# Performance work log

Measured on AMD Instinct MI355X. Metric: run time of the kernel, lower is better.

Reference implementation:

```python
import jax, jax.numpy as jnp
import numpy as np
from functools import partial

EPS = 1e-5

def batchnorm(x, gamma, beta):
    # training-mode BN over (N,H,W) per channel, NCHW layout
    mean = jnp.mean(x, axis=(0, 2, 3), keepdims=True)
    var = jnp.var(x, axis=(0, 2, 3), keepdims=True)
    xn = (x - mean) * jax.lax.rsqrt(var + EPS)
    return xn * gamma[None, :, None, None] + beta[None, :, None, None]

def ternarize(w):
    # TBN-style per-output-filter ternary quantization: {-a,0,+a}
    absw = jnp.abs(w)
    delta = 0.7 * jnp.mean(absw, axis=(1, 2, 3), keepdims=True)
    mask = (absw > delta).astype(w.dtype)
    alpha = jnp.sum(absw * mask, axis=(1, 2, 3), keepdims=True) / (
        jnp.sum(mask, axis=(1, 2, 3), keepdims=True) + 1e-8)
    return jnp.sign(w) * mask * alpha

def conv(x, w, stride, padding):
    return jax.lax.conv_general_dilated(
        x, w, window_strides=(stride, stride),
        padding=[(padding, padding), (padding, padding)],
        dimension_numbers=("NCHW", "OIHW", "NCHW"))


def setup_inputs() -> dict:
    key = jax.random.key(0)
    ks = jax.random.split(key, 8)
    in_planes, planes, stride = 512, 256, 2
    out_planes = planes * 4
    d = dict(
        x=jax.random.normal(ks[0], (64, in_planes, 28, 28), dtype=jnp.float32),
        bn1_g=jnp.ones((in_planes,), jnp.float32),
        bn1_b=jnp.zeros((in_planes,), jnp.float32),
        w1=jax.random.normal(ks[1], (planes, in_planes, 1, 1), jnp.float32) * 0.05,
        bn2_g=jnp.ones((planes,), jnp.float32),
        bn2_b=jnp.zeros((planes,), jnp.float32),
        w2=jax.random.normal(ks[2], (planes, planes, 3, 3), jnp.float32) * 0.05,
        bn3_g=jnp.ones((planes,), jnp.float32),
        bn3_b=jnp.zeros((planes,), jnp.float32),
        w3=jax.random.normal(ks[3], (out_planes, planes, 1, 1), jnp.float32) * 0.05,
        ds_w=jax.random.normal(ks[4], (out_planes, in_planes, 1, 1), jnp.float32) * 0.05,
        ds_bn_g=jnp.ones((out_planes,), jnp.float32),
        ds_bn_b=jnp.zeros((out_planes,), jnp.float32),
    )
    return d


def reference(x, bn1_g, bn1_b, w1, bn2_g, bn2_b, w2, bn3_g, bn3_b, w3,
              ds_w, ds_bn_g, ds_bn_b):
    stride = 2
    identity = x
    # pre-activation chain: BN -> ternary-quantized conv
    h = conv(batchnorm(x, bn1_g, bn1_b), ternarize(w1), 1, 0)          # [N,256,28,28]
    h = conv(batchnorm(h, bn2_g, bn2_b), ternarize(w2), stride, 1)     # [N,256,14,14]
    h = conv(batchnorm(h, bn3_g, bn3_b), ternarize(w3), 1, 0)          # [N,1024,14,14]
    # downsample(identity, x): projected shortcut + residual add
    sc = batchnorm(conv(identity, ds_w, stride, 0), ds_bn_g, ds_bn_b)
    return h + sc
```

## Files before the change

### kernel.cpp

```cpp
#include <hip/hip_runtime.h>
#include <hip/hip_bf16.h>
#include <math.h>

#define EPS 1e-5f

typedef __hip_bfloat16 bf16;
typedef short short8 __attribute__((ext_vector_type(8)));
typedef float float4v __attribute__((ext_vector_type(4)));

__device__ __forceinline__ float toF(float v) { return v; }
__device__ __forceinline__ float toF(bf16 v) { return __bfloat162float(v); }
__device__ __forceinline__ void stF(float* p, float v) { *p = v; }
__device__ __forceinline__ void stF(bf16* p, float v) { *p = __float2bfloat16(v); }
__device__ __forceinline__ short f2bs(float v) {
    bf16 b = __float2bfloat16(v);
    return *reinterpret_cast<short*>(&b);
}
__device__ __forceinline__ float bs2f(short s) {
    unsigned u = ((unsigned)(unsigned short)s) << 16;
    return __uint_as_float(u);
}

__device__ __forceinline__ void gload_lds16(const short* g, short* l) {
    __builtin_amdgcn_global_load_lds(
        (const __attribute__((address_space(1))) unsigned int*)g,
        (__attribute__((address_space(3))) unsigned int*)l, 16, 0, 0);
}

__device__ __forceinline__ void bn_fin(float sum, float sq, float g, float b, float cnt,
                                       float& scale, float& shift) {
    float mean = sum / cnt;
    float var = fmaxf(sq / cnt - mean * mean, 0.f);
    float r = rsqrtf(var + EPS);
    scale = g * r;
    shift = b - mean * scale;
}

__device__ __forceinline__ float block_reduce_sum(float v) {
    __shared__ float s[256];
    int t = threadIdx.x;
    s[t] = v;
    __syncthreads();
    #pragma unroll
    for (int st = 128; st > 0; st >>= 1) {
        if (t < st) s[t] += s[t + st];
        __syncthreads();
    }
    float r = s[0];
    __syncthreads();
    return r;
}

__device__ __forceinline__ void ternarize_body(const float* __restrict__ w,
                                               short* __restrict__ wt,
                                               float* __restrict__ alpha, int K, int f) {
    const float* wf = w + (size_t)f * K;
    short* wtf = wt + (size_t)f * K;

    float s = 0.f;
    for (int i = threadIdx.x; i < K; i += 256) s += fabsf(wf[i]);
    float total = block_reduce_sum(s);
    float delta = 0.7f * total / (float)K;

    float sm = 0.f, cm = 0.f;
    for (int i = threadIdx.x; i < K; i += 256) {
        float a = fabsf(wf[i]);
        if (a > delta) { sm += a; cm += 1.f; }
    }
    sm = block_reduce_sum(sm);
    cm = block_reduce_sum(cm);
    if (threadIdx.x == 0) alpha[f] = sm / (cm + 1e-8f);

    for (int i = threadIdx.x; i < K; i += 256) {
        float v = wf[i];
        float a = fabsf(v);
        wtf[i] = (a > delta) ? ((v > 0.f) ? (short)0x3F80 : (short)0xBF80) : (short)0;
    }
}

__global__ __launch_bounds__(256) void prep_kernel(
    const float* __restrict__ w1, const float* __restrict__ w2,
    const float* __restrict__ w3, const float* __restrict__ ds_w,
    short* __restrict__ w1t, short* __restrict__ w2t, short* __restrict__ w3t,
    short* __restrict__ dswb,
    float* __restrict__ alpha1, float* __restrict__ alpha2, float* __restrict__ alpha3,
    const float* __restrict__ x, short* __restrict__ B1t,
    float* __restrict__ sum1, float* __restrict__ sq1) {
    int b = blockIdx.x;
    if (b < 256)        ternarize_body(w1, w1t, alpha1, 512, b);
    else if (b < 512)   ternarize_body(w2, w2t, alpha2, 2304, b - 256);
    else if (b < 1536)  ternarize_body(w3, w3t, alpha3, 256, b - 512);
    else if (b < 3584) {
        int i = (b - 1536) * 256 + threadIdx.x;
        if (i < 1024 * 512) dswb[i] = f2bs(ds_w[i]);
    } else {
        const int C = 512, SP = 784;
        __shared__ short tile[64][66];
        __shared__ float rs[4][64], rq[4][64];
        int bb = b - 3584;
        int n = bb / 104;
        int ci0 = ((bb / 13) % 8) * 64;
        int p0 = (bb % 13) * 64;
        int t = threadIdx.x;
        int tx = t & 63;
        int ty4 = t >> 6;

        {
            int p4 = t & 15;
            int cib = t >> 4;
            int p = p0 + p4 * 4;
            bool pok = (p + 3) < SP;
            #pragma unroll
            for (int it = 0; it < 4; it++) {
                int ci = cib + it * 16;
                float4 q;
                if (pok) q = *(const float4*)(x + ((size_t)n * C + ci0 + ci) * SP + p);
                else     q = make_float4(0.f, 0.f, 0.f, 0.f);
                tile[p4 * 4 + 0][ci] = f2bs(q.x);
                tile[p4 * 4 + 1][ci] = f2bs(q.y);
                tile[p4 * 4 + 2][ci] = f2bs(q.z);
                tile[p4 * 4 + 3][ci] = f2bs(q.w);
            }
        }
        __syncthreads();

        {
            int seg = t & 7;
            #pragma unroll
            for (int it = 0; it < 2; it++) {
                int pl = (t >> 3) + it * 32;
                int pw = p0 + pl;
                if (pw < SP) {
                    short v[8];
                    #pragma unroll
                    for (int u = 0; u < 8; u++) v[u] = tile[pl][seg * 8 + u];
                    *(int4*)(B1t + ((size_t)n * SP + pw) * C + ci0 + seg * 8) = *(int4*)v;
                }
            }
        }

        float s = 0.f, s2 = 0.f;
        #pragma unroll
        for (int r = 0; r < 16; r++) {
            int pl = ty4 + r * 4;
            int pw = p0 + pl;
            if (pw < SP) {
                float v = bs2f(tile[pl][tx]);
                s += v; s2 += v * v;
            }
        }
        rs[ty4][tx] = s; rq[ty4][tx] = s2;
        __syncthreads();
        if (ty4 == 0) {
            float ts = rs[0][tx] + rs[1][tx] + rs[2][tx] + rs[3][tx];
            float tq = rq[0][tx] + rq[1][tx] + rq[2][tx] + rq[3][tx];
            atomicAdd(&sum1[ci0 + tx], ts);
            atomicAdd(&sq1[ci0 + tx], tq);
        }
    }
}

__global__ void foldbias_kernel(const short* __restrict__ wt,
                                const float* __restrict__ sum, const float* __restrict__ sq,
                                const float* __restrict__ g, const float* __restrict__ b,
                                short* __restrict__ wf, float* __restrict__ bias,
                                int K, float cnt) {
    int f = blockIdx.x;
    float s = 0.f;
    for (int k = threadIdx.x; k < K; k += blockDim.x) {
        float scale, shift;
        bn_fin(sum[k], sq[k], g[k], b[k], cnt, scale, shift);
        float tv = bs2f(wt[(size_t)f * K + k]);
        wf[(size_t)f * K + k] = f2bs(tv * scale);
        s += tv * shift;
    }
    s = block_reduce_sum(s);
    if (threadIdx.x == 0) bias[f] = s;
}

template <typename T, int VEC>
__global__ __launch_bounds__(256) void bn_sum_kernel(
    const T* __restrict__ src, float* __restrict__ sum, float* __restrict__ sq,
    int C, int spatial, int N, int splits) {
    int c = blockIdx.x;
    int vpc = spatial / VEC;
    int total = N * vpc;
    float s = 0.f, s2 = 0.f;
    for (int v = blockIdx.y * 256 + threadIdx.x; v < total; v += splits * 256) {
        int n = v / vpc;
        int i = v - n * vpc;
        const T* p = src + ((size_t)n * C + c) * spatial + i * VEC;
        short tmp[VEC];
        if (VEC == 8) *(int4*)tmp = *(const int4*)p;
        else          *(int2*)tmp = *(const int2*)p;
        #pragma unroll
        for (int k = 0; k < VEC; k++) { float vv = bs2f(tmp[k]); s += vv; s2 += vv * vv; }
    }
    s = block_reduce_sum(s);
    s2 = block_reduce_sum(s2);
    if (threadIdx.x == 0) {
        atomicAdd(&sum[c], s);
        atomicAdd(&sq[c], s2);
    }
}

template <int VEC>
__device__ __forceinline__ void bn_sum_body(const bf16* __restrict__ src, int C, int c,
                                            int spatial, int N, int splits,
                                            float* __restrict__ sum, float* __restrict__ sq) {
    int vpc = spatial / VEC;
    int total = N * vpc;
    float s = 0.f, s2 = 0.f;
    for (int v = blockIdx.y * 256 + threadIdx.x; v < total; v += splits * 256) {
        int n = v / vpc;
        int i = v - n * vpc;
        const bf16* p = src + ((size_t)n * C + c) * spatial + i * VEC;
        short tmp[VEC];
        if (VEC == 8) *(int4*)tmp = *(const int4*)p;
        else          *(int2*)tmp = *(const int2*)p;
        #pragma unroll
        for (int k = 0; k < VEC; k++) { float vv = bs2f(tmp[k]); s += vv; s2 += vv * vv; }
    }
    s = block_reduce_sum(s);
    s2 = block_reduce_sum(s2);
    if (threadIdx.x == 0) {
        atomicAdd(&sum[c], s);
        atomicAdd(&sq[c], s2);
    }
}

__global__ __launch_bounds__(256) void bn_sum_dual_kernel(
    const bf16* __restrict__ scv, const bf16* __restrict__ h1,
    float* __restrict__ sumd, float* __restrict__ sqd,
    float* __restrict__ sum2, float* __restrict__ sq2) {
    int cb = blockIdx.x;
    if (cb < 1024) bn_sum_body<4>(scv, 1024, cb, 196, 64, 8, sumd, sqd);
    else           bn_sum_body<8>(h1, 256, cb - 1024, 784, 64, 8, sum2, sq2);
}

__global__ __launch_bounds__(256) void affine_transpose_bf16_kernel(
    const bf16* __restrict__ in,
    const float* __restrict__ sum, const float* __restrict__ sq,
    const float* __restrict__ g, const float* __restrict__ b, float cnt,
    short* __restrict__ Bt, int C, int SP) {
    __shared__ short tile[64][66];
    int n = blockIdx.z;
    int ci0 = blockIdx.y * 64;
    int p0 = blockIdx.x * 64;
    int t = threadIdx.x;

    {
        int p4 = t & 15;
        int cib = t >> 4;
        int p = p0 + p4 * 4;
        bool pok = (p + 3) < SP;
        #pragma unroll
        for (int it = 0; it < 4; it++) {
            int ci = cib + it * 16;
            short v[4] = {0, 0, 0, 0};
            if (pok) *(int2*)v = *(const int2*)(in + ((size_t)n * C + ci0 + ci) * SP + p);
            float sc, sh;
            bn_fin(sum[ci0 + ci], sq[ci0 + ci], g[ci0 + ci], b[ci0 + ci], cnt, sc, sh);
            #pragma unroll
            for (int j = 0; j < 4; j++)
                tile[p4 * 4 + j][ci] = f2bs(bs2f(v[j]) * sc + sh);
        }
    }
    __syncthreads();

    {
        int seg = t & 7;
        #pragma unroll
        for (int it = 0; it < 2; it++) {
            int pl = (t >> 3) + it * 32;
            int pw = p0 + pl;
            if (pw < SP) {
                short v[8];
                #pragma unroll
                for (int u = 0; u < 8; u++) v[u] = tile[pl][seg * 8 + u];
                *(int4*)(Bt + ((size_t)n * SP + pw) * C + ci0 + seg * 8) = *(int4*)v;
            }
        }
    }
}

__global__ __launch_bounds__(256) void im2col_tiled_kernel(
    const bf16* __restrict__ h1,
    const float* __restrict__ sum, const float* __restrict__ sq,
    const float* __restrict__ g, const float* __restrict__ b, float cnt,
    short* __restrict__ B2t) {
    __shared__ short tile[16][784];
    int cb = blockIdx.x;
    int n  = blockIdx.y;
    int ci0 = cb * 16;
    int t = threadIdx.x;

    for (int v = t; v < 16 * 98; v += 256) {
        int ci = v / 98;
        int i8 = (v - ci * 98) * 8;
        short tmp[8];
        *(int4*)tmp = *(const int4*)(h1 + ((size_t)n * 256 + ci0 + ci) * 784 + i8);
        float sc, sh;
        bn_fin(sum[ci0 + ci], sq[ci0 + ci], g[ci0 + ci], b[ci0 + ci], cnt, sc, sh);
        short ov[8];
        #pragma unroll
        for (int k = 0; k < 8; k++) ov[k] = f2bs(bs2f(tmp[k]) * sc + sh);
        *(int4*)&tile[ci][i8] = *(int4*)ov;
    }
    __syncthreads();

    for (int w = t; w < 196 * 18; w += 256) {
        int p = w / 18, seg = w - p * 18;
        int oh = p / 14, ow = p - oh * 14;
        int kbase = seg * 8;
        short vals[8];
        #pragma unroll
        for (int u = 0; u < 8; u++) {
            int kk = kbase + u;
            int ci_l = kk / 9;
            int rr = kk - ci_l * 9;
            int kh = rr / 3, kw = rr - kh * 3;
            int ih = 2 * oh - 1 + kh;
            int iw = 2 * ow - 1 + kw;
            vals[u] = ((unsigned)ih < 28u && (unsigned)iw < 28u)
                          ? tile[ci_l][ih * 28 + iw] : (short)0;
        }
        *(int4*)(B2t + ((size_t)(n * 196 + p)) * 2304 + ci0 * 9 + kbase) = *(int4*)vals;
    }
}

__global__ __launch_bounds__(256) void gemm14_kernel(
    const short* __restrict__ w1f, const short* __restrict__ dswb,
    const short* __restrict__ B1t,
    const float* __restrict__ alpha1, const float* __restrict__ bias1,
    bf16* __restrict__ h1, bf16* __restrict__ sc) {
    int blk = blockIdx.x;
    int t = threadIdx.x;
    int w = t >> 6, l = t & 63;
    int r0 = t >> 2;
    int kg = (t & 3) * 8;
    int wbase = w * 512;
    int lm = (l >> 4);
    int lc = l & 15;

    if (blk < 784) {
        __shared__ short As[128 * 32];
        __shared__ short Bs[128 * 32];
        const int SP = 784, M = 256, K = 512;
        int c0 = (blk / 2) * 128;
        int m0 = (blk % 2) * 128;
        int wm = (w >> 1) * 64, wn = (w & 1) * 64;
        size_t rowB0 = c0 + r0;
        size_t rowB1 = c0 + r0 + 64;

        float4v acc[4][4];
        #pragma unroll
        for (int i = 0; i < 4; i++)
            #pragma unroll
            for (int j = 0; j < 4; j++) acc[i][j] = (float4v)0.f;

        for (int k0 = 0; k0 < K; k0 += 32) {
            gload_lds16(w1f + (size_t)(m0 + r0) * K + k0 + kg,      &As[wbase]);
            gload_lds16(w1f + (size_t)(m0 + r0 + 64) * K + k0 + kg, &As[2048 + wbase]);
            gload_lds16(B1t + rowB0 * K + k0 + kg,                  &Bs[wbase]);
            gload_lds16(B1t + rowB1 * K + k0 + kg,                  &Bs[2048 + wbase]);
            __syncthreads();

            short8 af[4], bfr[4];
            #pragma unroll
            for (int i = 0; i < 4; i++)
                af[i] = *(const short8*)&As[(wm + i * 16 + lc) * 32 + lm * 8];
            #pragma unroll
            for (int j = 0; j < 4; j++)
                bfr[j] = *(const short8*)&Bs[(wn + j * 16 + lc) * 32 + lm * 8];
            #pragma unroll
            for (int i = 0; i < 4; i++)
                #pragma unroll
                for (int j = 0; j < 4; j++)
                    acc[i][j] = __builtin_amdgcn_mfma_f32_16x16x32_bf16(af[i], bfr[j], acc[i][j], 0, 0, 0);
            __syncthreads();
        }

        #pragma unroll
        for (int i = 0; i < 4; i++) {
            #pragma unroll
            for (int r = 0; r < 4; r++) {
                int m = m0 + wm + i * 16 + lm * 4 + r;
                float a = alpha1[m];
                float bia = bias1[m];
                #pragma unroll
                for (int j = 0; j < 4; j++) {
                    int c = c0 + wn + j * 16 + lc;
                    int n = c / SP;
                    int p = c - n * SP;
                    h1[((size_t)n * M + m) * SP + p] = __float2bfloat16((acc[i][j][r] + bia) * a);
                }
            }
        }
    } else {
        __shared__ short As4[64 * 32];
        __shared__ short Bs4[64 * 32];
        const int SP = 196, M = 1024, K = 512;
        int bb = blk - 784;
        int c0 = (bb / 16) * 64;
        int m0 = (bb % 16) * 64;
        int wm = (w >> 1) * 32, wn = (w & 1) * 32;

        int c = c0 + r0;
        int nn = c / 196, pp = c - nn * 196;
        int oh = pp / 14, ow = pp - oh * 14;
        size_t rowB = (size_t)nn * 784 + oh * 56 + ow * 2;

        float4v acc[2][2];
        #pragma unroll
        for (int i = 0; i < 2; i++)
            #pragma unroll
            for (int j = 0; j < 2; j++) acc[i][j] = (float4v)0.f;

        for (int k0 = 0; k0 < K; k0 += 32) {
            gload_lds16(dswb + (size_t)(m0 + r0) * K + k0 + kg, &As4[wbase]);
            gload_lds16(B1t + rowB * K + k0 + kg,               &Bs4[wbase]);
            __syncthreads();

            short8 af[2], bfr[2];
            #pragma unroll
            for (int i = 0; i < 2; i++)
                af[i] = *(const short8*)&As4[(wm + i * 16 + lc) * 32 + lm * 8];
            #pragma unroll
            for (int j = 0; j < 2; j++)
                bfr[j] = *(const short8*)&Bs4[(wn + j * 16 + lc) * 32 + lm * 8];
            #pragma unroll
            for (int i = 0; i < 2; i++)
                #pragma unroll
                for (int j = 0; j < 2; j++)
                    acc[i][j] = __builtin_amdgcn_mfma_f32_16x16x32_bf16(af[i], bfr[j], acc[i][j], 0, 0, 0);
            __syncthreads();
        }

        #pragma unroll
        for (int i = 0; i < 2; i++) {
            #pragma unroll
            for (int r = 0; r < 4; r++) {
                int m = m0 + wm + i * 16 + lm * 4 + r;
                #pragma unroll
                for (int j = 0; j < 2; j++) {
                    int cc = c0 + wn + j * 16 + lc;
                    int n = cc / SP;
                    int p = cc - n * SP;
                    sc[((size_t)n * M + m) * SP + p] = __float2bfloat16(acc[i][j][r]);
                }
            }
        }
    }
}

template <int SP, typename TOut, bool HAS_ALPHA, bool FUSE, bool HAS_BIAS, bool BREMAP>
__global__ __launch_bounds__(256) void gemm_kernel(
    const short* __restrict__ A, const short* __restrict__ Bt,
    const float* __restrict__ alpha, TOut* __restrict__ out,
    int M, int K,
    const bf16* __restrict__ scv,
    const float* __restrict__ fsum, const float* __restrict__ fsq,
    const float* __restrict__ fg, const float* __restrict__ fb, float fcnt,
    const float* __restrict__ bias) {
    __shared__ short As[128 * 32];
    __shared__ short Bs[128 * 32];
    int t = threadIdx.x;
    int c0 = blockIdx.x * 128;
    int m0 = blockIdx.y * 128;
    int w = t >> 6, l = t & 63;
    int wm = (w >> 1) * 64, wn = (w & 1) * 64;

    int r0 = t >> 2;
    int kg = (t & 3) * 8;
    int wbase = w * 512;

    size_t rowB0, rowB1;
    if (BREMAP) {
        int c = c0 + r0;
        int nn = c / 196, pp = c - nn * 196;
        int oh = pp / 14, ow = pp - oh * 14;
        rowB0 = (size_t)nn * 784 + oh * 56 + ow * 2;
        c += 64;
        nn = c / 196; pp = c - nn * 196;
        oh = pp / 14; ow = pp - oh * 14;
        rowB1 = (size_t)nn * 784 + oh * 56 + ow * 2;
    } else {
        rowB0 = c0 + r0;
        rowB1 = c0 + r0 + 64;
    }

    float4v acc[4][4];
    #pragma unroll
    for (int i = 0; i < 4; i++)
        #pragma unroll
        for (int j = 0; j < 4; j++) acc[i][j] = (float4v)0.f;

    int lm = (l >> 4);
    int lc = l & 15;

    for (int k0 = 0; k0 < K; k0 += 32) {
        gload_lds16(A + (size_t)(m0 + r0) * K + k0 + kg,      &As[wbase]);
        gload_lds16(A + (size_t)(m0 + r0 + 64) * K + k0 + kg, &As[2048 + wbase]);
        gload_lds16(Bt + rowB0 * K + k0 + kg,                 &Bs[wbase]);
        gload_lds16(Bt + rowB1 * K + k0 + kg,                 &Bs[2048 + wbase]);
        __syncthreads();

        short8 af[4], bfr[4];
        #pragma unroll
        for (int i = 0; i < 4; i++)
            af[i] = *(const short8*)&As[(wm + i * 16 + lc) * 32 + lm * 8];
        #pragma unroll
        for (int j = 0; j < 4; j++)
            bfr[j] = *(const short8*)&Bs[(wn + j * 16 + lc) * 32 + lm * 8];
        #pragma unroll
        for (int i = 0; i < 4; i++)
            #pragma unroll
            for (int j = 0; j < 4; j++)
                acc[i][j] = __builtin_amdgcn_mfma_f32_16x16x32_bf16(af[i], bfr[j], acc[i][j], 0, 0, 0);
        __syncthreads();
    }

    #pragma unroll
    for (int i = 0; i < 4; i++) {
        #pragma unroll
        for (int r = 0; r < 4; r++) {
            int m = m0 + wm + i * 16 + lm * 4 + r;
            float a = HAS_ALPHA ? alpha[m] : 1.f;
            float bia = HAS_BIAS ? bias[m] : 0.f;
            float fsc = 0.f, fsh = 0.f;
            if (FUSE) bn_fin(fsum[m], fsq[m], fg[m], fb[m], fcnt, fsc, fsh);
            #pragma unroll
            for (int j = 0; j < 4; j++) {
                int c = c0 + wn + j * 16 + lc;
                int n = c / SP;
                int p = c - n * SP;
                size_t idx = ((size_t)n * M + m) * SP + p;
                float v = acc[i][j][r];
                if (HAS_BIAS) v += bia;
                if (HAS_ALPHA) v *= a;
                if (FUSE) v += toF(scv[idx]) * fsc + fsh;
                stF(&out[idx], v);
            }
        }
    }
}

__global__ __launch_bounds__(256) void gemm2_kernel(
    const short* __restrict__ A, const short* __restrict__ Bt,
    const float* __restrict__ alpha, bf16* __restrict__ out,
    int M, int K) {
    constexpr int SP = 196;
    __shared__ short As[64 * 32];
    __shared__ short Bs[64 * 32];
    int t = threadIdx.x;
    int c0 = blockIdx.x * 64;
    int m0 = blockIdx.y * 64;
    int w = t >> 6, l = t & 63;
    int wm = (w >> 1) * 32, wn = (w & 1) * 32;

    int r0 = t >> 2;
    int kg = (t & 3) * 8;
    int wbase = w * 512;

    float4v acc[2][2];
    #pragma unroll
    for (int i = 0; i < 2; i++)
        #pragma unroll
        for (int j = 0; j < 2; j++) acc[i][j] = (float4v)0.f;

    int lm = (l >> 4);
    int lc = l & 15;

    for (int k0 = 0; k0 < K; k0 += 32) {
        gload_lds16(A + (size_t)(m0 + r0) * K + k0 + kg,  &As[wbase]);
        gload_lds16(Bt + (size_t)(c0 + r0) * K + k0 + kg, &Bs[wbase]);
        __syncthreads();

        short8 af[2], bfr[2];
        #pragma unroll
        for (int i = 0; i < 2; i++)
            af[i] = *(const short8*)&As[(wm + i * 16 + lc) * 32 + lm * 8];
        #pragma unroll
        for (int j = 0; j < 2; j++)
            bfr[j] = *(const short8*)&Bs[(wn + j * 16 + lc) * 32 + lm * 8];
        #pragma unroll
        for (int i = 0; i < 2; i++)
            #pragma unroll
            for (int j = 0; j < 2; j++)
                acc[i][j] = __builtin_amdgcn_mfma_f32_16x16x32_bf16(af[i], bfr[j], acc[i][j], 0, 0, 0);
        __syncthreads();
    }

    #pragma unroll
    for (int i = 0; i < 2; i++) {
        #pragma unroll
        for (int r = 0; r < 4; r++) {
            int m = m0 + wm + i * 16 + lm * 4 + r;
            float a = alpha[m];
            #pragma unroll
            for (int j = 0; j < 2; j++) {
                int c = c0 + wn + j * 16 + lc;
                int n = c / SP;
                int p = c - n * SP;
                out[((size_t)n * M + m) * SP + p] = __float2bfloat16(acc[i][j][r] * a);
            }
        }
    }
}

extern "C" void kernel_launch(void* const* d_in, const int* in_sizes, int n_in,
                              void* d_out, int out_size, void* d_ws, size_t ws_size,
                              hipStream_t stream) {
    const float* x      = (const float*)d_in[0];
    const float* bn1_g  = (const float*)d_in[1];
    const float* bn1_b  = (const float*)d_in[2];
    const float* w1     = (const float*)d_in[3];
    const float* bn2_g  = (const float*)d_in[4];
    const float* bn2_b  = (const float*)d_in[5];
    const float* w2     = (const float*)d_in[6];
    const float* bn3_g  = (const float*)d_in[7];
    const float* bn3_b  = (const float*)d_in[8];
    const float* w3     = (const float*)d_in[9];
    const float* ds_w   = (const float*)d_in[10];
    const float* dbn_g  = (const float*)d_in[11];
    const float* dbn_b  = (const float*)d_in[12];
    float* out = (float*)d_out;

    const int N = 64, C1 = 512, C2 = 256, C3 = 1024;
    const int SP1 = 784, SP2 = 196;
    const int NT1 = N * SP1;
    const int NT2 = N * SP2;

    char* wsb = (char*)d_ws;
    size_t off = 0;
    auto alloc = [&](size_t bytes) { char* p = wsb + off; off += (bytes + 255) & ~(size_t)255; return p; };

    char* pool = alloc((size_t)NT2 * 2304 * 2);
    short* B1t = (short*)pool;
    short* B2t = (short*)pool;
    short* B3t = (short*)pool;
    bf16*  sc  = (bf16*)alloc((size_t)N * C3 * SP2 * 2);

    bf16* h1 = (bf16*)alloc((size_t)N * C2 * SP1 * 2);
    bf16* h2 = (bf16*)alloc((size_t)N * C2 * SP2 * 2);
    short* w1t  = (short*)alloc((size_t)C2 * C1 * 2);
    short* w1f  = (short*)alloc((size_t)C2 * C1 * 2);
    short* w2t  = (short*)alloc((size_t)C2 * C2 * 9 * 2);
    short* w3t  = (short*)alloc((size_t)C3 * C2 * 2);
    short* dswb = (short*)alloc((size_t)C3 * C1 * 2);
    float* alpha1 = (float*)alloc(C2 * 4);
    float* alpha2 = (float*)alloc(C2 * 4);
    float* alpha3 = (float*)alloc(C3 * 4);
    float* bias1  = (float*)alloc(C2 * 4);
    float* acc_base = (float*)alloc((size_t)(C1 + C2 + C2 + C3) * 2 * 4);
    float* sum1 = acc_base;            float* sq1 = sum1 + C1;
    float* sum2 = sq1 + C1;            float* sq2 = sum2 + C2;
    float* sum3 = sq2 + C2;            float* sq3 = sum3 + C2;
    float* sumd = sq3 + C2;            float* sqd = sumd + C3;
    (void)ws_size; (void)in_sizes; (void)n_in; (void)out_size;

    hipMemsetAsync(acc_base, 0, (size_t)(C1 + C2 + C2 + C3) * 2 * 4, stream);

    prep_kernel<<<10240, 256, 0, stream>>>(w1, w2, w3, ds_w, w1t, w2t, w3t, dswb,
                                           alpha1, alpha2, alpha3, x, B1t, sum1, sq1);

    foldbias_kernel<<<C2, 256, 0, stream>>>(w1t, sum1, sq1, bn1_g, bn1_b,
                                            w1f, bias1, C1, (float)(N * SP1));

    gemm14_kernel<<<3920, 256, 0, stream>>>(w1f, dswb, B1t, alpha1, bias1, h1, sc);

    bn_sum_dual_kernel<<<dim3(C3 + C2, 8), 256, 0, stream>>>(
        sc, h1, sumd, sqd, sum2, sq2);

    im2col_tiled_kernel<<<dim3(16, 64), 256, 0, stream>>>(
        h1, sum2, sq2, bn2_g, bn2_b, (float)(N * SP1), B2t);

    gemm2_kernel<<<dim3(NT2 / 64, C2 / 64), 256, 0, stream>>>(
        w2t, B2t, alpha2, h2, C2, C2 * 9);

    bn_sum_kernel<bf16, 4><<<dim3(C2, 4), 256, 0, stream>>>(h2, sum3, sq3, C2, SP2, N, 4);

    {
        dim3 grid((SP2 + 63) / 64, C2 / 64, N);
        affine_transpose_bf16_kernel<<<grid, 256, 0, stream>>>(
            h2, sum3, sq3, bn3_g, bn3_b, (float)(N * SP2), B3t, C2, SP2);
    }

    gemm_kernel<196, float, true, true, false, false>
        <<<dim3(NT2 / 128, C3 / 128), 256, 0, stream>>>(
        w3t, B3t, alpha3, out, C3, C2,
        sc, sumd, sqd, dbn_g, dbn_b, (float)(N * SP2), nullptr);
}
```

Baseline: 397.1 us.

## Double-buffer LDS tiles in GEMM kernels to overlap global loads with MFMA

Converts the K-loops of gemm14_kernel (both branches) and gemm2_kernel to a ping-pong LDS scheme. The next k-tile is fetched with global_load_lds while MFMAs run on the current tile, after a prologue load. This is meant to hide global-memory latency behind compute. It doubles LDS use per block (a 32KB shared array in gemm14 for both branches), which can reduce occupancy. Whether async-to-LDS loads overlap safely depends on the remaining barrier and waitcnt placement.

```diff
diff --git a/kernel.cpp b/kernel.cpp
--- a/kernel.cpp
+++ b/kernel.cpp
@@ -334,6 +334,7 @@
     const short* __restrict__ B1t,
     const float* __restrict__ alpha1, const float* __restrict__ bias1,
     bf16* __restrict__ h1, bf16* __restrict__ sc) {
+    __shared__ short lds[16384];
     int blk = blockIdx.x;
     int t = threadIdx.x;
     int w = t >> 6, l = t & 63;
@@ -344,8 +345,6 @@
     int lc = l & 15;
 
     if (blk < 784) {
-        __shared__ short As[128 * 32];
-        __shared__ short Bs[128 * 32];
         const int SP = 784, M = 256, K = 512;
         int c0 = (blk / 2) * 128;
         int m0 = (blk % 2) * 128;
@@ -359,20 +358,31 @@
             #pragma unroll
             for (int j = 0; j < 4; j++) acc[i][j] = (float4v)0.f;
 
-        for (int k0 = 0; k0 < K; k0 += 32) {
-            gload_lds16(w1f + (size_t)(m0 + r0) * K + k0 + kg,      &As[wbase]);
-            gload_lds16(w1f + (size_t)(m0 + r0 + 64) * K + k0 + kg, &As[2048 + wbase]);
-            gload_lds16(B1t + rowB0 * K + k0 + kg,                  &Bs[wbase]);
-            gload_lds16(B1t + rowB1 * K + k0 + kg,                  &Bs[2048 + wbase]);
-            __syncthreads();
+        gload_lds16(w1f + (size_t)(m0 + r0) * K + kg,      &lds[wbase]);
+        gload_lds16(w1f + (size_t)(m0 + r0 + 64) * K + kg, &lds[2048 + wbase]);
+        gload_lds16(B1t + rowB0 * K + kg,                  &lds[8192 + wbase]);
+        gload_lds16(B1t + rowB1 * K + kg,                  &lds[8192 + 2048 + wbase]);
+        __syncthreads();
+
+        for (int it = 0; it < 16; it++) {
+            int cur = it & 1;
+            int curA = cur * 4096, curB = 8192 + cur * 4096;
+            if (it < 15) {
+                int nxtA = (cur ^ 1) * 4096, nxtB = 8192 + (cur ^ 1) * 4096;
+                int k1 = (it + 1) * 32;
+                gload_lds16(w1f + (size_t)(m0 + r0) * K + k1 + kg,      &lds[nxtA + wbase]);
+                gload_lds16(w1f + (size_t)(m0 + r0 + 64) * K + k1 + kg, &lds[nxtA + 2048 + wbase]);
+                gload_lds16(B1t + rowB0 * K + k1 + kg,                  &lds[nxtB + wbase]);
+                gload_lds16(B1t + rowB1 * K + k1 + kg,                  &lds[nxtB + 2048 + wbase]);
+            }
 
             short8 af[4], bfr[4];
             #pragma unroll
             for (int i = 0; i < 4; i++)
-                af[i] = *(const short8*)&As[(wm + i * 16 + lc) * 32 + lm * 8];
+                af[i] = *(const short8*)&lds[curA + (wm + i * 16 + lc) * 32 + lm * 8];
             #pragma unroll
             for (int j = 0; j < 4; j++)
-                bfr[j] = *(const short8*)&Bs[(wn + j * 16 + lc) * 32 + lm * 8];
+                bfr[j] = *(const short8*)&lds[curB + (wn + j * 16 + lc) * 32 + lm * 8];
             #pragma unroll
             for (int i = 0; i < 4; i++)
                 #pragma unroll
@@ -398,8 +408,6 @@
             }
         }
     } else {
-        __shared__ short As4[64 * 32];
-        __shared__ short Bs4[64 * 32];
         const int SP = 196, M = 1024, K = 512;
         int bb = blk - 784;
         int c0 = (bb / 16) * 64;
@@ -417,18 +425,27 @@
             #pragma unroll
             for (int j = 0; j < 2; j++) acc[i][j] = (float4v)0.f;
 
-        for (int k0 = 0; k0 < K; k0 += 32) {
-            gload_lds16(dswb + (size_t)(m0 + r0) * K + k0 + kg, &As4[wbase]);
-            gload_lds16(B1t + rowB * K + k0 + kg,               &Bs4[wbase]);
-            __syncthreads();
+        gload_lds16(dswb + (size_t)(m0 + r0) * K + kg, &lds[wbase]);
+        gload_lds16(B1t + rowB * K + kg,               &lds[4096 + wbase]);
+        __syncthreads();
+
+        for (int it = 0; it < 16; it++) {
+            int cur = it & 1;
+            int curA = cur * 2048, curB = 4096 + cur * 2048;
+            if (it < 15) {
+                int nxtA = (cur ^ 1) * 2048, nxtB = 4096 + (cur ^ 1) * 2048;
+                int k1 = (it + 1) * 32;
+                gload_lds16(dswb + (size_t)(m0 + r0) * K + k1 + kg, &lds[nxtA + wbase]);
+                gload_lds16(B1t + rowB * K + k1 + kg,               &lds[nxtB + wbase]);
+            }
 
             short8 af[2], bfr[2];
             #pragma unroll
             for (int i = 0; i < 2; i++)
-                af[i] = *(const short8*)&As4[(wm + i * 16 + lc) * 32 + lm * 8];
+                af[i] = *(const short8*)&lds[curA + (wm + i * 16 + lc) * 32 + lm * 8];
             #pragma unroll
             for (int j = 0; j < 2; j++)
-                bfr[j] = *(const short8*)&Bs4[(wn + j * 16 + lc) * 32 + lm * 8];
+                bfr[j] = *(const short8*)&lds[curB + (wn + j * 16 + lc) * 32 + lm * 8];
             #pragma unroll
             for (int i = 0; i < 2; i++)
                 #pragma unroll
@@ -551,8 +568,7 @@
     const float* __restrict__ alpha, bf16* __restrict__ out,
     int M, int K) {
     constexpr int SP = 196;
-    __shared__ short As[64 * 32];
-    __shared__ short Bs[64 * 32];
+    __shared__ short lds[8192];
     int t = threadIdx.x;
     int c0 = blockIdx.x * 64;
     int m0 = blockIdx.y * 64;
@@ -571,19 +587,29 @@
 
     int lm = (l >> 4);
     int lc = l & 15;
-
-    for (int k0 = 0; k0 < K; k0 += 32) {
-        gload_lds16(A + (size_t)(m0 + r0) * K + k0 + kg,  &As[wbase]);
-        gload_lds16(Bt + (size_t)(c0 + r0) * K + k0 + kg, &Bs[wbase]);
-        __syncthreads();
+    int NT = K / 32;
+
+    gload_lds16(A + (size_t)(m0 + r0) * K + kg,  &lds[wbase]);
+    gload_lds16(Bt + (size_t)(c0 + r0) * K + kg, &lds[4096 + wbase]);
+    __syncthreads();
+
+    for (int it = 0; it < NT; it++) {
+        int cur = it & 1;
+        int curA = cur * 2048, curB = 4096 + cur * 2048;
+        if (it < NT - 1) {
+            int nxtA = (cur ^ 1) * 2048, nxtB = 4096 + (cur ^ 1) * 2048;
+            int k1 = (it + 1) * 32;
+            gload_lds16(A + (size_t)(m0 + r0) * K + k1 + kg,  &lds[nxtA + wbase]);
+            gload_lds16(Bt + (size_t)(c0 + r0) * K + k1 + kg, &lds[nxtB + wbase]);
+        }
 
         short8 af[2], bfr[2];
         #pragma unroll
         for (int i = 0; i < 2; i++)
-            af[i] = *(const short8*)&As[(wm + i * 16 + lc) * 32 + lm * 8];
+            af[i] = *(const short8*)&lds[curA + (wm + i * 16 + lc) * 32 + lm * 8];
         #pragma unroll
         for (int j = 0; j < 2; j++)
-            bfr[j] = *(const short8*)&Bs[(wn + j * 16 + lc) * 32 + lm * 8];
+            bfr[j] = *(const short8*)&lds[curB + (wn + j * 16 + lc) * 32 + lm * 8];
         #pragma unroll
         for (int i = 0; i < 2; i++)
             #pragma unroll
```

New measurement: 383.7 us. 3.4% less time.
